# Kernel optimization log

Measured on AMD Instinct MI355X. Metric: run time of the kernel, lower is better.

## Reference

```python
import jax, jax.numpy as jnp
import numpy as np

CLIP_LIMIT = 10.0
NTILES = 8        # OpenCV createCLAHE default tileGridSize=(8,8)
NBINS = 256

_M_RGB2XYZ = jnp.array([[0.412453, 0.357580, 0.180423],
                        [0.212671, 0.715160, 0.072169],
                        [0.019334, 0.119193, 0.950227]], dtype=jnp.float32)
_M_XYZ2RGB = jnp.array([[ 3.240479, -1.537150, -0.498535],
                        [-0.969256,  1.875992,  0.041556],
                        [ 0.055648, -0.204043,  1.057311]], dtype=jnp.float32)
_WP = jnp.array([0.950456, 1.0, 1.088754], dtype=jnp.float32)  # D65 white point (OpenCV)
_EPS = 0.008856


def rgb2lab(rgb):  # rgb: [H,W,3] in [0,1]
    xyz = jnp.einsum('hwc,dc->hwd', rgb, _M_RGB2XYZ) / _WP
    f = jnp.where(xyz > _EPS, jnp.cbrt(xyz), 7.787 * xyz + 16.0 / 116.0)
    fx, fy, fz = f[..., 0], f[..., 1], f[..., 2]
    L = 116.0 * fy - 16.0
    a = 500.0 * (fx - fy)
    b = 200.0 * (fy - fz)
    return L, a, b


def lab2rgb(L, a, b):
    fy = (L + 16.0) / 116.0
    fx = fy + a / 500.0
    fz = fy - b / 200.0
    f = jnp.stack([fx, fy, fz], axis=-1)
    xyz = jnp.where(f ** 3 > _EPS, f ** 3, (f - 16.0 / 116.0) / 7.787) * _WP
    rgb = jnp.einsum('hwd,cd->hwc', xyz, _M_XYZ2RGB)
    return jnp.clip(rgb, 0.0, 1.0)


def clahe_channel(L8, clip_limit):
    # L8: [H,W] int32 in [0,255]
    H, W = L8.shape
    th, tw = H // NTILES, W // NTILES
    area = float(th * tw)
    # per-tile histograms via one scatter-add
    rows = jnp.arange(H) // th            # [H] tile row id
    cols = jnp.arange(W) // tw            # [W] tile col id
    tid = rows[:, None] * NTILES + cols[None, :]          # [H,W]
    flat = (tid * NBINS + L8).ravel()
    hist = jnp.zeros(NTILES * NTILES * NBINS, jnp.float32).at[flat].add(1.0)
    hist = hist.reshape(NTILES * NTILES, NBINS)
    # clip + uniform redistribution of excess
    clip = max(clip_limit * area / NBINS, 1.0)
    excess = jnp.sum(jnp.maximum(hist - clip, 0.0), axis=1, keepdims=True)
    hist = jnp.minimum(hist, clip) + excess / NBINS
    # CDF -> LUT (OpenCV: lutScale = 255/tileArea, rounded)
    cdf = jnp.cumsum(hist, axis=1)
    lut = jnp.clip(jnp.round(cdf * (255.0 / area)), 0.0, 255.0)  # [T, 256]
    # bilinear interpolation between tile LUTs
    fy = jnp.clip((jnp.arange(H, dtype=jnp.float32) + 0.5) / th - 0.5, 0.0, NTILES - 1.0)
    fx = jnp.clip((jnp.arange(W, dtype=jnp.float32) + 0.5) / tw - 0.5, 0.0, NTILES - 1.0)
    y0 = jnp.floor(fy).astype(jnp.int32); y1 = jnp.minimum(y0 + 1, NTILES - 1)
    x0 = jnp.floor(fx).astype(jnp.int32); x1 = jnp.minimum(x0 + 1, NTILES - 1)
    wy = (fy - y0)[:, None]; wx = (fx - x0)[None, :]
    def g(yi, xi):  # gather LUT value for each pixel from tile (yi, xi)
        return lut[yi[:, None] * NTILES + xi[None, :], L8]
    top = (1.0 - wx) * g(y0, x0) + wx * g(y0, x1)
    bot = (1.0 - wx) * g(y1, x0) + wx * g(y1, x1)
    return (1.0 - wy) * top + wy * bot   # [H,W] float in [0,255]


def setup_inputs() -> dict:
    key = jax.random.key(0)
    x = jax.random.uniform(key, (3, 2048, 2048), dtype=jnp.float32)
    return {"x": x}


def reference(x) -> jnp.ndarray:
    hwc = jnp.transpose(x, (1, 2, 0))          # CHW -> HWC
    L, a, b = rgb2lab(hwc)                      # L in [0,100]
    L8 = jnp.clip(jnp.round(L * (255.0 / 100.0)), 0, 255).astype(jnp.int32)
    L_eq = clahe_channel(L8, CLIP_LIMIT) * (100.0 / 255.0)
    rgb = lab2rgb(L_eq, a, b)
    return jnp.transpose(rgb, (2, 0, 1))        # HWC -> CHW
```

## Files before the change

### kernel.cpp

```cpp
#include <hip/hip_runtime.h>
#include <stdint.h>

#define HW 4194304
#define WIDTH 2048
#define F(x) ((float)(x))

__device__ __forceinline__ float cbrtf_glibc(float x) {
    unsigned int bits = __float_as_uint(x);
    int xe = (int)((bits >> 23) & 0xFF) - 126;
    float xm = __uint_as_float((bits & 0x007FFFFFu) | 0x3F000000u);

    static const double factor[5] = {
        1.0 / 1.5874010519681994748,
        1.0 / 1.2599210498948731648,
        1.0,
        1.2599210498948731648,
        1.5874010519681994748
    };

    double xmd = (double)xm;
    double p = __dsub_rn(0.697570460207922770, __dmul_rn(0.191502161678719066, xmd));
    p = __dadd_rn(0.492659620528969547, __dmul_rn(p, xmd));
    float u = (float)p;

    float t2 = __fmul_rn(__fmul_rn(u, u), u);

    double ud  = (double)u;
    double t2d = (double)t2;
    double num = __dmul_rn(ud, __dadd_rn(t2d, __dmul_rn(2.0, xmd)));
    double den = __dadd_rn(__dmul_rn(2.0, t2d), xmd);
    double ym  = __dmul_rn(__ddiv_rn(num, den), factor[2 + (xe % 3)]);
    float ymf = (float)ym;

    return ldexpf(ymf, xe / 3);
}

__device__ __forceinline__ void rgb2lab_px(float r, float g, float b,
                                           int& l8, float& A_, float& B_) {
    float X = __fadd_rn(__fadd_rn(__fmul_rn(r, F(0.412453)), __fmul_rn(g, F(0.357580))), __fmul_rn(b, F(0.180423)));
    float Y = __fadd_rn(__fadd_rn(__fmul_rn(r, F(0.212671)), __fmul_rn(g, F(0.715160))), __fmul_rn(b, F(0.072169)));
    float Z = __fadd_rn(__fadd_rn(__fmul_rn(r, F(0.019334)), __fmul_rn(g, F(0.119193))), __fmul_rn(b, F(0.950227)));
    X = __fdiv_rn(X, F(0.950456));
    Z = __fdiv_rn(Z, F(1.088754));
    const float EPS = F(0.008856);
    const float C0  = F(16.0 / 116.0);
    float fx = (X > EPS) ? cbrtf_glibc(X) : __fadd_rn(__fmul_rn(F(7.787), X), C0);
    float fy = (Y > EPS) ? cbrtf_glibc(Y) : __fadd_rn(__fmul_rn(F(7.787), Y), C0);
    float fz = (Z > EPS) ? cbrtf_glibc(Z) : __fadd_rn(__fmul_rn(F(7.787), Z), C0);
    float L  = __fsub_rn(__fmul_rn(F(116.0), fy), F(16.0));
    A_ = __fmul_rn(F(500.0), __fsub_rn(fx, fy));
    B_ = __fmul_rn(F(200.0), __fsub_rn(fy, fz));
    float Lr = rintf(__fmul_rn(L, F(255.0 / 100.0)));
    Lr = fminf(fmaxf(Lr, 0.0f), 255.0f);
    l8 = (int)Lr;
}

__global__ __launch_bounds__(256) void k_hist(const float* __restrict__ x,
        unsigned int* __restrict__ hist,
        float2* __restrict__ ab_out,
        unsigned char* __restrict__ l8_out, int store) {
    __shared__ unsigned int h[2048];
    const int t = threadIdx.x;
    const int y = blockIdx.x;
    #pragma unroll
    for (int i = 0; i < 8; ++i) h[i * 256 + t] = 0;
    __syncthreads();
    const float* R  = x;
    const float* G  = x + HW;
    const float* Bp = x + 2 * HW;
    const int rowbase = y * WIDTH;
    #pragma unroll
    for (int c = 0; c < 8; ++c) {
        int col = c * 256 + t;
        int idx = rowbase + col;
        float r = R[idx], g = G[idx], b = Bp[idx];
        int l8; float A_, B_;
        rgb2lab_px(r, g, b, l8, A_, B_);
        if (store) {
            ab_out[idx] = make_float2(A_, B_);
            l8_out[idx] = (unsigned char)l8;
        }
        atomicAdd(&h[((col >> 8) << 8) + l8], 1u);
    }
    __syncthreads();
    const int tilerow = y >> 8;
    unsigned int* gh = hist + tilerow * 2048;
    #pragma unroll
    for (int i = 0; i < 8; ++i) {
        unsigned int v = h[i * 256 + t];
        if (v) atomicAdd(&gh[i * 256 + t], v);
    }
}

__global__ __launch_bounds__(256) void k_lut(const unsigned int* __restrict__ hist,
                                             float* __restrict__ lut) {
    __shared__ float sh[256];
    __shared__ float hc[256];
    const int t = threadIdx.x;
    const int tile = blockIdx.x;
    float h = (float)hist[tile * 256 + t];
    sh[t] = fmaxf(h - 2560.0f, 0.0f);
    __syncthreads();
    for (int s = 128; s > 0; s >>= 1) {
        if (t < s) sh[t] += sh[t + s];
        __syncthreads();
    }
    float excess = sh[0];
    hc[t] = __fadd_rn(fminf(h, 2560.0f), __fmul_rn(excess, F(1.0 / 256.0)));
    __syncthreads();
    if (t == 0) {
        float c = 0.0f;
        for (int i = 0; i < 256; ++i) { c = __fadd_rn(c, hc[i]); hc[i] = c; }
    }
    __syncthreads();
    float v = rintf(__fmul_rn(hc[t], F(255.0 / 65536.0)));
    lut[tile * 256 + t] = fminf(fmaxf(v, 0.0f), 255.0f);
}

__global__ __launch_bounds__(256) void k_apply(const float* __restrict__ x,
        const float* __restrict__ lut,
        const float2* __restrict__ ab_in,
        const unsigned char* __restrict__ l8_in,
        float* __restrict__ out, int stored) {
    __shared__ float lutS[4096];
    const int t = threadIdx.x;
    const int y = blockIdx.x;

    float fyc = fminf(fmaxf(((float)y + 0.5f) * (1.0f / 256.0f) - 0.5f, 0.0f), 7.0f);
    int y0 = (int)floorf(fyc); int y1 = min(y0 + 1, 7);
    float wy = __fsub_rn(fyc, (float)y0);
    float omwy = __fsub_rn(1.0f, wy);

    const float* ltop = lut + y0 * 2048;
    const float* lbot = lut + y1 * 2048;
    #pragma unroll
    for (int i = 0; i < 8; ++i) {
        lutS[i * 256 + t]        = ltop[i * 256 + t];
        lutS[2048 + i * 256 + t] = lbot[i * 256 + t];
    }
    __syncthreads();

    const int rowbase = y * WIDTH;
    #pragma unroll
    for (int c = 0; c < 8; ++c) {
        int col = c * 256 + t;
        int idx = rowbase + col;
        int l8; float A_, B_;
        if (stored) {
            float2 ab = ab_in[idx];
            A_ = ab.x; B_ = ab.y;
            l8 = (int)l8_in[idx];
        } else {
            float r = x[idx], g = x[idx + HW], b = x[idx + 2 * HW];
            rgb2lab_px(r, g, b, l8, A_, B_);
        }
        float fxc = fminf(fmaxf(((float)col + 0.5f) * (1.0f / 256.0f) - 0.5f, 0.0f), 7.0f);
        int x0 = (int)floorf(fxc); int x1 = min(x0 + 1, 7);
        float wx = __fsub_rn(fxc, (float)x0);
        float omwx = __fsub_rn(1.0f, wx);
        float g00 = lutS[x0 * 256 + l8];
        float g01 = lutS[x1 * 256 + l8];
        float g10 = lutS[2048 + x0 * 256 + l8];
        float g11 = lutS[2048 + x1 * 256 + l8];
        float top = __fadd_rn(__fmul_rn(omwx, g00), __fmul_rn(wx, g01));
        float bot = __fadd_rn(__fmul_rn(omwx, g10), __fmul_rn(wx, g11));
        float Leq = __fmul_rn(__fadd_rn(__fmul_rn(omwy, top), __fmul_rn(wy, bot)),
                              F(100.0 / 255.0));
        const float EPS = F(0.008856);
        const float C0  = F(16.0 / 116.0);
        float fy2 = __fdiv_rn(__fadd_rn(Leq, 16.0f), 116.0f);
        float fx2 = __fadd_rn(fy2, __fdiv_rn(A_, 500.0f));
        float fz2 = __fsub_rn(fy2, __fdiv_rn(B_, 200.0f));
        float t3;
        t3 = fx2 * fx2 * fx2;
        float X = ((t3 > EPS) ? t3 : __fdiv_rn(__fsub_rn(fx2, C0), F(7.787))) * F(0.950456);
        t3 = fy2 * fy2 * fy2;
        float Y = ((t3 > EPS) ? t3 : __fdiv_rn(__fsub_rn(fy2, C0), F(7.787))) * F(1.0);
        t3 = fz2 * fz2 * fz2;
        float Z = ((t3 > EPS) ? t3 : __fdiv_rn(__fsub_rn(fz2, C0), F(7.787))) * F(1.088754);
        float rr = __fadd_rn(__fadd_rn(__fmul_rn(X, F(3.240479)),  __fmul_rn(Y, F(-1.537150))), __fmul_rn(Z, F(-0.498535)));
        float gg = __fadd_rn(__fadd_rn(__fmul_rn(X, F(-0.969256)), __fmul_rn(Y, F(1.875992))),  __fmul_rn(Z, F(0.041556)));
        float bb = __fadd_rn(__fadd_rn(__fmul_rn(X, F(0.055648)),  __fmul_rn(Y, F(-0.204043))), __fmul_rn(Z, F(1.057311)));
        rr = fminf(fmaxf(rr, 0.0f), 1.0f);
        gg = fminf(fmaxf(gg, 0.0f), 1.0f);
        bb = fminf(fmaxf(bb, 0.0f), 1.0f);
        out[idx]          = rr;
        out[idx + HW]     = gg;
        out[idx + 2 * HW] = bb;
    }
}

extern "C" void kernel_launch(void* const* d_in, const int* in_sizes, int n_in,
                              void* d_out, int out_size, void* d_ws, size_t ws_size,
                              hipStream_t stream) {
    const float* x = (const float*)d_in[0];
    float* out = (float*)d_out;
    char* ws = (char*)d_ws;
    unsigned int* hist = (unsigned int*)ws;
    float* lut = (float*)(ws + 65536);
    const size_t off = 131072;
    float2* ab_buf = (float2*)(ws + off);
    unsigned char* l8_buf = (unsigned char*)(ws + off + (size_t)HW * 8);
    const size_t need = off + (size_t)HW * 9;
    const int store = (ws_size >= need) ? 1 : 0;

    (void)hipMemsetAsync(hist, 0, 65536, stream);
    k_hist<<<2048, 256, 0, stream>>>(x, hist, ab_buf, l8_buf, store);
    k_lut<<<64, 256, 0, stream>>>(hist, lut);
    k_apply<<<2048, 256, 0, stream>>>(x, lut, ab_buf, l8_buf, out, store);
}
```

Measured before the change: 134.4 us.

## Fuse histogram, LUT and apply into one cooperative kernel with register-held Lab

Replaces the three-kernel pipeline with a single cooperative kernel of 1024 blocks. Each block handles two rows and keeps the a/b values and packed L8 in registers across two grid-wide syncs, so the 36 MB intermediate write and re-read through the workspace disappears. The LUT prefix sum becomes a parallel Hillis-Steele scan instead of a serial loop. In exchange it adds grid-sync cost and register pressure under launch_bounds(256,4), and depends on all 1024 blocks being co-resident, falling back to the old path otherwise.

```diff
diff --git a/kernel.cpp b/kernel.cpp
--- a/kernel.cpp
+++ b/kernel.cpp
@@ -1,5 +1,8 @@
 #include <hip/hip_runtime.h>
+#include <hip/hip_cooperative_groups.h>
 #include <stdint.h>
+
+namespace cg = cooperative_groups;
 
 #define HW 4194304
 #define WIDTH 2048
@@ -55,6 +58,153 @@
     l8 = (int)Lr;
 }
 
+__device__ __forceinline__ void lab2rgb_store(float Leq, float A_, float B_,
+                                              float* __restrict__ out, int idx) {
+    const float EPS = F(0.008856);
+    const float C0  = F(16.0 / 116.0);
+    float fy2 = __fdiv_rn(__fadd_rn(Leq, 16.0f), 116.0f);
+    float fx2 = __fadd_rn(fy2, __fdiv_rn(A_, 500.0f));
+    float fz2 = __fsub_rn(fy2, __fdiv_rn(B_, 200.0f));
+    float t3;
+    t3 = fx2 * fx2 * fx2;
+    float X = ((t3 > EPS) ? t3 : __fdiv_rn(__fsub_rn(fx2, C0), F(7.787))) * F(0.950456);
+    t3 = fy2 * fy2 * fy2;
+    float Y = ((t3 > EPS) ? t3 : __fdiv_rn(__fsub_rn(fy2, C0), F(7.787))) * F(1.0);
+    t3 = fz2 * fz2 * fz2;
+    float Z = ((t3 > EPS) ? t3 : __fdiv_rn(__fsub_rn(fz2, C0), F(7.787))) * F(1.088754);
+    float rr = __fadd_rn(__fadd_rn(__fmul_rn(X, F(3.240479)),  __fmul_rn(Y, F(-1.537150))), __fmul_rn(Z, F(-0.498535)));
+    float gg = __fadd_rn(__fadd_rn(__fmul_rn(X, F(-0.969256)), __fmul_rn(Y, F(1.875992))),  __fmul_rn(Z, F(0.041556)));
+    float bb = __fadd_rn(__fadd_rn(__fmul_rn(X, F(0.055648)),  __fmul_rn(Y, F(-0.204043))), __fmul_rn(Z, F(1.057311)));
+    rr = fminf(fmaxf(rr, 0.0f), 1.0f);
+    gg = fminf(fmaxf(gg, 0.0f), 1.0f);
+    bb = fminf(fmaxf(bb, 0.0f), 1.0f);
+    out[idx]          = rr;
+    out[idx + HW]     = gg;
+    out[idx + 2 * HW] = bb;
+}
+
+__global__ __launch_bounds__(256, 4) void k_fused(
+        const float* __restrict__ x,
+        unsigned int* __restrict__ hist,
+        float* __restrict__ lut,
+        float* __restrict__ out) {
+    __shared__ float lds[4096];
+    const int t = threadIdx.x;
+    const int b = blockIdx.x;
+    const int r0 = b * 2;
+
+    unsigned int* h = (unsigned int*)lds;
+    #pragma unroll
+    for (int i = 0; i < 8; ++i) h[i * 256 + t] = 0;
+    __syncthreads();
+
+    const float* R  = x;
+    const float* G  = x + HW;
+    const float* Bp = x + 2 * HW;
+
+    float Areg[2][8], Breg[2][8];
+    unsigned int l8p[2][2] = {{0u, 0u}, {0u, 0u}};
+
+    #pragma unroll
+    for (int rr = 0; rr < 2; ++rr) {
+        const int rowbase = (r0 + rr) * WIDTH;
+        #pragma unroll
+        for (int c = 0; c < 8; ++c) {
+            int col = c * 256 + t;
+            int idx = rowbase + col;
+            float r = R[idx], g = G[idx], bb = Bp[idx];
+            int l8; float A_, B_;
+            rgb2lab_px(r, g, bb, l8, A_, B_);
+            Areg[rr][c] = A_;
+            Breg[rr][c] = B_;
+            l8p[rr][c >> 2] |= (unsigned int)l8 << ((c & 3) * 8);
+            atomicAdd(&h[((col >> 8) << 8) + l8], 1u);
+        }
+    }
+    __syncthreads();
+    {
+        const int tilerow = r0 >> 8;
+        unsigned int* gh = hist + tilerow * 2048;
+        #pragma unroll
+        for (int i = 0; i < 8; ++i) {
+            unsigned int v = h[i * 256 + t];
+            if (v) atomicAdd(&gh[i * 256 + t], v);
+        }
+    }
+    __threadfence();
+    cg::this_grid().sync();
+
+    if (b < 64) {
+        float hval = (float)hist[b * 256 + t];
+        float* sh = lds;
+        sh[t] = fmaxf(hval - 2560.0f, 0.0f);
+        __syncthreads();
+        for (int s = 128; s > 0; s >>= 1) {
+            if (t < s) sh[t] += sh[t + s];
+            __syncthreads();
+        }
+        float excess = sh[0];
+        float val = __fadd_rn(fminf(hval, 2560.0f), __fmul_rn(excess, F(1.0 / 256.0)));
+        float* sc = lds + 256;
+        sc[t] = val;
+        __syncthreads();
+        #pragma unroll
+        for (int s = 1; s < 256; s <<= 1) {
+            float add = (t >= s) ? sc[t - s] : 0.0f;
+            __syncthreads();
+            val = __fadd_rn(val, add);
+            sc[t] = val;
+            __syncthreads();
+        }
+        float lv = rintf(__fmul_rn(val, F(255.0 / 65536.0)));
+        lut[b * 256 + t] = fminf(fmaxf(lv, 0.0f), 255.0f);
+    }
+    cg::this_grid().sync();
+
+    float fyc = fminf(fmaxf(((float)r0 + 0.5f) * (1.0f / 256.0f) - 0.5f, 0.0f), 7.0f);
+    int y0 = (int)floorf(fyc);
+    int y1 = min(y0 + 1, 7);
+    const float* ltop = lut + y0 * 2048;
+    const float* lbot = lut + y1 * 2048;
+    #pragma unroll
+    for (int i = 0; i < 8; ++i) {
+        lds[i * 256 + t]        = ltop[i * 256 + t];
+        lds[2048 + i * 256 + t] = lbot[i * 256 + t];
+    }
+    __syncthreads();
+
+    #pragma unroll
+    for (int rr = 0; rr < 2; ++rr) {
+        const int y = r0 + rr;
+        float fyr = fminf(fmaxf(((float)y + 0.5f) * (1.0f / 256.0f) - 0.5f, 0.0f), 7.0f);
+        float wy = __fsub_rn(fyr, (float)y0);
+        float omwy = __fsub_rn(1.0f, wy);
+        const int rowbase = y * WIDTH;
+        #pragma unroll
+        for (int c = 0; c < 8; ++c) {
+            int col = c * 256 + t;
+            int idx = rowbase + col;
+            int l8 = (int)((l8p[rr][c >> 2] >> ((c & 3) * 8)) & 0xFFu);
+            float A_ = Areg[rr][c];
+            float B_ = Breg[rr][c];
+            float fxc = fminf(fmaxf(((float)col + 0.5f) * (1.0f / 256.0f) - 0.5f, 0.0f), 7.0f);
+            int x0 = (int)floorf(fxc);
+            int x1 = min(x0 + 1, 7);
+            float wx = __fsub_rn(fxc, (float)x0);
+            float omwx = __fsub_rn(1.0f, wx);
+            float g00 = lds[x0 * 256 + l8];
+            float g01 = lds[x1 * 256 + l8];
+            float g10 = lds[2048 + x0 * 256 + l8];
+            float g11 = lds[2048 + x1 * 256 + l8];
+            float top = __fadd_rn(__fmul_rn(omwx, g00), __fmul_rn(wx, g01));
+            float bot = __fadd_rn(__fmul_rn(omwx, g10), __fmul_rn(wx, g11));
+            float Leq = __fmul_rn(__fadd_rn(__fmul_rn(omwy, top), __fmul_rn(wy, bot)),
+                                  F(100.0 / 255.0));
+            lab2rgb_store(Leq, A_, B_, out, idx);
+        }
+    }
+}
+
 __global__ __launch_bounds__(256) void k_hist(const float* __restrict__ x,
         unsigned int* __restrict__ hist,
         float2* __restrict__ ab_out,
@@ -166,27 +316,7 @@
         float bot = __fadd_rn(__fmul_rn(omwx, g10), __fmul_rn(wx, g11));
         float Leq = __fmul_rn(__fadd_rn(__fmul_rn(omwy, top), __fmul_rn(wy, bot)),
                               F(100.0 / 255.0));
-        const float EPS = F(0.008856);
-        const float C0  = F(16.0 / 116.0);
-        float fy2 = __fdiv_rn(__fadd_rn(Leq, 16.0f), 116.0f);
-        float fx2 = __fadd_rn(fy2, __fdiv_rn(A_, 500.0f));
-        float fz2 = __fsub_rn(fy2, __fdiv_rn(B_, 200.0f));
-        float t3;
-        t3 = fx2 * fx2 * fx2;
-        float X = ((t3 > EPS) ? t3 : __fdiv_rn(__fsub_rn(fx2, C0), F(7.787))) * F(0.950456);
-        t3 = fy2 * fy2 * fy2;
-        float Y = ((t3 > EPS) ? t3 : __fdiv_rn(__fsub_rn(fy2, C0), F(7.787))) * F(1.0);
-        t3 = fz2 * fz2 * fz2;
-        float Z = ((t3 > EPS) ? t3 : __fdiv_rn(__fsub_rn(fz2, C0), F(7.787))) * F(1.088754);
-        float rr = __fadd_rn(__fadd_rn(__fmul_rn(X, F(3.240479)),  __fmul_rn(Y, F(-1.537150))), __fmul_rn(Z, F(-0.498535)));
-        float gg = __fadd_rn(__fadd_rn(__fmul_rn(X, F(-0.969256)), __fmul_rn(Y, F(1.875992))),  __fmul_rn(Z, F(0.041556)));
-        float bb = __fadd_rn(__fadd_rn(__fmul_rn(X, F(0.055648)),  __fmul_rn(Y, F(-0.204043))), __fmul_rn(Z, F(1.057311)));
-        rr = fminf(fmaxf(rr, 0.0f), 1.0f);
-        gg = fminf(fmaxf(gg, 0.0f), 1.0f);
-        bb = fminf(fmaxf(bb, 0.0f), 1.0f);
-        out[idx]          = rr;
-        out[idx + HW]     = gg;
-        out[idx + 2 * HW] = bb;
+        lab2rgb_store(Leq, A_, B_, out, idx);
     }
 }
 
@@ -198,14 +328,37 @@
     char* ws = (char*)d_ws;
     unsigned int* hist = (unsigned int*)ws;
     float* lut = (float*)(ws + 65536);
-    const size_t off = 131072;
-    float2* ab_buf = (float2*)(ws + off);
-    unsigned char* l8_buf = (unsigned char*)(ws + off + (size_t)HW * 8);
-    const size_t need = off + (size_t)HW * 9;
-    const int store = (ws_size >= need) ? 1 : 0;
+
+    static int coop_state = -1;
+    if (coop_state < 0) {
+        int nb = 0, ncu = 0, dev = 0;
+        (void)hipGetDevice(&dev);
+        hipError_t e1 = hipOccupancyMaxActiveBlocksPerMultiprocessor(&nb, k_fused, 256, 0);
+        hipError_t e2 = hipDeviceGetAttribute(&ncu, hipDeviceAttributeMultiprocessorCount, dev);
+        coop_state = (e1 == hipSuccess && e2 == hipSuccess && nb * ncu >= 1024) ? 1 : 0;
+    }
 
     (void)hipMemsetAsync(hist, 0, 65536, stream);
-    k_hist<<<2048, 256, 0, stream>>>(x, hist, ab_buf, l8_buf, store);
-    k_lut<<<64, 256, 0, stream>>>(hist, lut);
-    k_apply<<<2048, 256, 0, stream>>>(x, lut, ab_buf, l8_buf, out, store);
-}
+
+    bool done = false;
+    if (coop_state == 1) {
+        const float* xa = x; unsigned int* ha = hist; float* la = lut; float* oa = out;
+        void* kargs[] = { (void*)&xa, (void*)&ha, (void*)&la, (void*)&oa };
+        hipError_t le = hipLaunchCooperativeKernel((const void*)k_fused,
+                                                   dim3(1024), dim3(256),
+                                                   kargs, 0u, stream);
+        done = (le == hipSuccess);
+        if (!done) coop_state = 0;
+    }
+
+    if (!done) {
+        const size_t off = 131072;
+        float2* ab_buf = (float2*)(ws + off);
+        unsigned char* l8_buf = (unsigned char*)(ws + off + (size_t)HW * 8);
+        const size_t need = off + (size_t)HW * 9;
+        const int store = (ws_size >= need) ? 1 : 0;
+        k_hist<<<2048, 256, 0, stream>>>(x, hist, ab_buf, l8_buf, store);
+        k_lut<<<64, 256, 0, stream>>>(hist, lut);
+        k_apply<<<2048, 256, 0, stream>>>(x, lut, ab_buf, l8_buf, out, store);
+    }
+}
```

Result: no change. 135.7 us (+0.9%).

## Fuse histogram, LUT, and apply into one persistent kernel with grid barrier

Applied to the files above, without the earlier changes.

Replaces the three-kernel pipeline with a single kernel. Each row block computes Lab in registers, builds its histogram, then waits at a software grid-wide barrier. After the barrier it builds only the two needed tile-row LUTs locally with wave shuffles and applies them without reloading pixels. This removes the intermediate a/b and L8 buffers in global memory and two kernel launches. In exchange it needs all 2048 blocks co-resident, which is checked via occupancy at runtime with a fallback path. Every block also redundantly recomputes 16 tile LUTs, and the spin barrier adds contention.

```diff
diff --git a/kernel.cpp b/kernel.cpp
--- a/kernel.cpp
+++ b/kernel.cpp
@@ -3,6 +3,7 @@
 
 #define HW 4194304
 #define WIDTH 2048
+#define NBLK 2048
 #define F(x) ((float)(x))
 
 __device__ __forceinline__ float cbrtf_glibc(float x) {
@@ -55,6 +56,162 @@
     l8 = (int)Lr;
 }
 
+__device__ __forceinline__ void lab2rgb_store(float Leq, float A_, float B_,
+                                              float* __restrict__ out, int idx) {
+    const float EPS = F(0.008856);
+    const float C0  = F(16.0 / 116.0);
+    float fy2 = __fdiv_rn(__fadd_rn(Leq, 16.0f), 116.0f);
+    float fx2 = __fadd_rn(fy2, __fdiv_rn(A_, 500.0f));
+    float fz2 = __fsub_rn(fy2, __fdiv_rn(B_, 200.0f));
+    float t3;
+    t3 = fx2 * fx2 * fx2;
+    float X = ((t3 > EPS) ? t3 : __fdiv_rn(__fsub_rn(fx2, C0), F(7.787))) * F(0.950456);
+    t3 = fy2 * fy2 * fy2;
+    float Y = ((t3 > EPS) ? t3 : __fdiv_rn(__fsub_rn(fy2, C0), F(7.787))) * F(1.0);
+    t3 = fz2 * fz2 * fz2;
+    float Z = ((t3 > EPS) ? t3 : __fdiv_rn(__fsub_rn(fz2, C0), F(7.787))) * F(1.088754);
+    float rr = __fadd_rn(__fadd_rn(__fmul_rn(X, F(3.240479)),  __fmul_rn(Y, F(-1.537150))), __fmul_rn(Z, F(-0.498535)));
+    float gg = __fadd_rn(__fadd_rn(__fmul_rn(X, F(-0.969256)), __fmul_rn(Y, F(1.875992))),  __fmul_rn(Z, F(0.041556)));
+    float bb = __fadd_rn(__fadd_rn(__fmul_rn(X, F(0.055648)),  __fmul_rn(Y, F(-0.204043))), __fmul_rn(Z, F(1.057311)));
+    rr = fminf(fmaxf(rr, 0.0f), 1.0f);
+    gg = fminf(fmaxf(gg, 0.0f), 1.0f);
+    bb = fminf(fmaxf(bb, 0.0f), 1.0f);
+    out[idx]          = rr;
+    out[idx + HW]     = gg;
+    out[idx + 2 * HW] = bb;
+}
+
+__global__ __launch_bounds__(256, 8) void k_fused_row(
+        const float* __restrict__ x,
+        unsigned int* __restrict__ hist,
+        unsigned int* __restrict__ bar,
+        float* __restrict__ out) {
+    __shared__ float lutS[4096];
+    unsigned int* h = (unsigned int*)lutS;
+    const int t = threadIdx.x;
+    const int y = blockIdx.x;
+
+    #pragma unroll
+    for (int i = 0; i < 8; ++i) h[i * 256 + t] = 0;
+    __syncthreads();
+
+    float A[8], B[8];
+    unsigned int l8p[2] = {0u, 0u};
+    const int rowbase = y * WIDTH;
+    #pragma unroll
+    for (int c = 0; c < 8; ++c) {
+        int col = c * 256 + t;
+        int idx = rowbase + col;
+        float r = x[idx], g = x[idx + HW], b = x[idx + 2 * HW];
+        int l8;
+        rgb2lab_px(r, g, b, l8, A[c], B[c]);
+        l8p[c >> 2] |= (unsigned int)l8 << ((c & 3) * 8);
+        atomicAdd(&h[((col >> 8) << 8) + l8], 1u);
+    }
+    __syncthreads();
+    {
+        unsigned int* gh = hist + (y >> 8) * 2048;
+        #pragma unroll
+        for (int i = 0; i < 8; ++i) {
+            unsigned int v = h[i * 256 + t];
+            if (v) atomicAdd(&gh[i * 256 + t], v);
+        }
+    }
+
+    __syncthreads();
+    if (t == 0) {
+        __threadfence();
+        unsigned int arrived = __hip_atomic_fetch_add(&bar[0], 1u,
+                                   __ATOMIC_ACQ_REL, __HIP_MEMORY_SCOPE_AGENT);
+        if (arrived == NBLK - 1) {
+            __hip_atomic_store(&bar[1], 1u, __ATOMIC_RELEASE, __HIP_MEMORY_SCOPE_AGENT);
+        } else {
+            for (long it = 0; it < (1L << 26); ++it) {
+                if (__hip_atomic_load(&bar[1], __ATOMIC_ACQUIRE,
+                                      __HIP_MEMORY_SCOPE_AGENT) != 0u) break;
+                __builtin_amdgcn_s_sleep(2);
+            }
+        }
+    }
+    __syncthreads();
+
+    float fyc = fminf(fmaxf(((float)y + 0.5f) * (1.0f / 256.0f) - 0.5f, 0.0f), 7.0f);
+    int y0 = (int)floorf(fyc);
+    int y1 = min(y0 + 1, 7);
+    float wy = __fsub_rn(fyc, (float)y0);
+    float omwy = __fsub_rn(1.0f, wy);
+
+    {
+        const int lane = t & 63;
+        const int w = t >> 6;
+        #pragma unroll
+        for (int i = 0; i < 4; ++i) {
+            int gidx = w * 4 + i;
+            int trow = gidx >> 3;
+            int tcol = gidx & 7;
+            int tile = (trow ? y1 : y0) * 8 + tcol;
+            const unsigned int* hp = hist + tile * 256 + lane * 4;
+            float h0 = (float)__hip_atomic_load(&hp[0], __ATOMIC_RELAXED, __HIP_MEMORY_SCOPE_AGENT);
+            float h1 = (float)__hip_atomic_load(&hp[1], __ATOMIC_RELAXED, __HIP_MEMORY_SCOPE_AGENT);
+            float h2 = (float)__hip_atomic_load(&hp[2], __ATOMIC_RELAXED, __HIP_MEMORY_SCOPE_AGENT);
+            float h3 = (float)__hip_atomic_load(&hp[3], __ATOMIC_RELAXED, __HIP_MEMORY_SCOPE_AGENT);
+            float e = __fadd_rn(__fadd_rn(fmaxf(h0 - 2560.0f, 0.0f),
+                                          fmaxf(h1 - 2560.0f, 0.0f)),
+                                __fadd_rn(fmaxf(h2 - 2560.0f, 0.0f),
+                                          fmaxf(h3 - 2560.0f, 0.0f)));
+            #pragma unroll
+            for (int d = 1; d < 64; d <<= 1) e = __fadd_rn(e, __shfl_xor(e, d));
+            float ex = __fmul_rn(e, F(1.0 / 256.0));
+            float v0 = __fadd_rn(fminf(h0, 2560.0f), ex);
+            float v1 = __fadd_rn(fminf(h1, 2560.0f), ex);
+            float v2 = __fadd_rn(fminf(h2, 2560.0f), ex);
+            float v3 = __fadd_rn(fminf(h3, 2560.0f), ex);
+            float s0 = v0;
+            float s1 = __fadd_rn(s0, v1);
+            float s2 = __fadd_rn(s1, v2);
+            float s3 = __fadd_rn(s2, v3);
+            float sc = s3;
+            #pragma unroll
+            for (int d = 1; d < 64; d <<= 1) {
+                float u2 = __shfl_up(sc, d);
+                if (lane >= d) sc = __fadd_rn(sc, u2);
+            }
+            float excl = __fsub_rn(sc, s3);
+            int base = trow * 2048 + tcol * 256 + lane * 4;
+            float c0 = rintf(__fmul_rn(__fadd_rn(excl, s0), F(255.0 / 65536.0)));
+            float c1 = rintf(__fmul_rn(__fadd_rn(excl, s1), F(255.0 / 65536.0)));
+            float c2 = rintf(__fmul_rn(__fadd_rn(excl, s2), F(255.0 / 65536.0)));
+            float c3 = rintf(__fmul_rn(__fadd_rn(excl, s3), F(255.0 / 65536.0)));
+            lutS[base + 0] = fminf(fmaxf(c0, 0.0f), 255.0f);
+            lutS[base + 1] = fminf(fmaxf(c1, 0.0f), 255.0f);
+            lutS[base + 2] = fminf(fmaxf(c2, 0.0f), 255.0f);
+            lutS[base + 3] = fminf(fmaxf(c3, 0.0f), 255.0f);
+        }
+    }
+    __syncthreads();
+
+    #pragma unroll
+    for (int c = 0; c < 8; ++c) {
+        int col = c * 256 + t;
+        int idx = rowbase + col;
+        int l8 = (int)((l8p[c >> 2] >> ((c & 3) * 8)) & 0xFFu);
+        float fxc = fminf(fmaxf(((float)col + 0.5f) * (1.0f / 256.0f) - 0.5f, 0.0f), 7.0f);
+        int x0 = (int)floorf(fxc);
+        int x1 = min(x0 + 1, 7);
+        float wx = __fsub_rn(fxc, (float)x0);
+        float omwx = __fsub_rn(1.0f, wx);
+        float g00 = lutS[x0 * 256 + l8];
+        float g01 = lutS[x1 * 256 + l8];
+        float g10 = lutS[2048 + x0 * 256 + l8];
+        float g11 = lutS[2048 + x1 * 256 + l8];
+        float top = __fadd_rn(__fmul_rn(omwx, g00), __fmul_rn(wx, g01));
+        float bot = __fadd_rn(__fmul_rn(omwx, g10), __fmul_rn(wx, g11));
+        float Leq = __fmul_rn(__fadd_rn(__fmul_rn(omwy, top), __fmul_rn(wy, bot)),
+                              F(100.0 / 255.0));
+        lab2rgb_store(Leq, A[c], B[c], out, idx);
+    }
+}
+
 __global__ __launch_bounds__(256) void k_hist(const float* __restrict__ x,
         unsigned int* __restrict__ hist,
         float2* __restrict__ ab_out,
@@ -65,15 +222,12 @@
     #pragma unroll
     for (int i = 0; i < 8; ++i) h[i * 256 + t] = 0;
     __syncthreads();
-    const float* R  = x;
-    const float* G  = x + HW;
-    const float* Bp = x + 2 * HW;
     const int rowbase = y * WIDTH;
     #pragma unroll
     for (int c = 0; c < 8; ++c) {
         int col = c * 256 + t;
         int idx = rowbase + col;
-        float r = R[idx], g = G[idx], b = Bp[idx];
+        float r = x[idx], g = x[idx + HW], b = x[idx + 2 * HW];
         int l8; float A_, B_;
         rgb2lab_px(r, g, b, l8, A_, B_);
         if (store) {
@@ -166,27 +320,7 @@
         float bot = __fadd_rn(__fmul_rn(omwx, g10), __fmul_rn(wx, g11));
         float Leq = __fmul_rn(__fadd_rn(__fmul_rn(omwy, top), __fmul_rn(wy, bot)),
                               F(100.0 / 255.0));
-        const float EPS = F(0.008856);
-        const float C0  = F(16.0 / 116.0);
-        float fy2 = __fdiv_rn(__fadd_rn(Leq, 16.0f), 116.0f);
-        float fx2 = __fadd_rn(fy2, __fdiv_rn(A_, 500.0f));
-        float fz2 = __fsub_rn(fy2, __fdiv_rn(B_, 200.0f));
-        float t3;
-        t3 = fx2 * fx2 * fx2;
-        float X = ((t3 > EPS) ? t3 : __fdiv_rn(__fsub_rn(fx2, C0), F(7.787))) * F(0.950456);
-        t3 = fy2 * fy2 * fy2;
-        float Y = ((t3 > EPS) ? t3 : __fdiv_rn(__fsub_rn(fy2, C0), F(7.787))) * F(1.0);
-        t3 = fz2 * fz2 * fz2;
-        float Z = ((t3 > EPS) ? t3 : __fdiv_rn(__fsub_rn(fz2, C0), F(7.787))) * F(1.088754);
-        float rr = __fadd_rn(__fadd_rn(__fmul_rn(X, F(3.240479)),  __fmul_rn(Y, F(-1.537150))), __fmul_rn(Z, F(-0.498535)));
-        float gg = __fadd_rn(__fadd_rn(__fmul_rn(X, F(-0.969256)), __fmul_rn(Y, F(1.875992))),  __fmul_rn(Z, F(0.041556)));
-        float bb = __fadd_rn(__fadd_rn(__fmul_rn(X, F(0.055648)),  __fmul_rn(Y, F(-0.204043))), __fmul_rn(Z, F(1.057311)));
-        rr = fminf(fmaxf(rr, 0.0f), 1.0f);
-        gg = fminf(fmaxf(gg, 0.0f), 1.0f);
-        bb = fminf(fmaxf(bb, 0.0f), 1.0f);
-        out[idx]          = rr;
-        out[idx + HW]     = gg;
-        out[idx + 2 * HW] = bb;
+        lab2rgb_store(Leq, A_, B_, out, idx);
     }
 }
 
@@ -197,15 +331,30 @@
     float* out = (float*)d_out;
     char* ws = (char*)d_ws;
     unsigned int* hist = (unsigned int*)ws;
+    unsigned int* bar  = (unsigned int*)(ws + 65536);
     float* lut = (float*)(ws + 65536);
-    const size_t off = 131072;
-    float2* ab_buf = (float2*)(ws + off);
-    unsigned char* l8_buf = (unsigned char*)(ws + off + (size_t)HW * 8);
-    const size_t need = off + (size_t)HW * 9;
-    const int store = (ws_size >= need) ? 1 : 0;
-
-    (void)hipMemsetAsync(hist, 0, 65536, stream);
-    k_hist<<<2048, 256, 0, stream>>>(x, hist, ab_buf, l8_buf, store);
-    k_lut<<<64, 256, 0, stream>>>(hist, lut);
-    k_apply<<<2048, 256, 0, stream>>>(x, lut, ab_buf, l8_buf, out, store);
-}
+
+    static int fused_ok = -1;
+    if (fused_ok < 0) {
+        int nb = 0, ncu = 0, dev = 0;
+        (void)hipGetDevice(&dev);
+        hipError_t e1 = hipOccupancyMaxActiveBlocksPerMultiprocessor(&nb, k_fused_row, 256, 0);
+        hipError_t e2 = hipDeviceGetAttribute(&ncu, hipDeviceAttributeMultiprocessorCount, dev);
+        fused_ok = (e1 == hipSuccess && e2 == hipSuccess && nb * ncu >= NBLK) ? 1 : 0;
+    }
+
+    (void)hipMemsetAsync(ws, 0, 65536 + 64, stream);
+
+    if (fused_ok == 1) {
+        k_fused_row<<<NBLK, 256, 0, stream>>>(x, hist, bar, out);
+    } else {
+        const size_t off = 131072;
+        float2* ab_buf = (float2*)(ws + off);
+        unsigned char* l8_buf = (unsigned char*)(ws + off + (size_t)HW * 8);
+        const size_t need = off + (size_t)HW * 9;
+        const int store = (ws_size >= need) ? 1 : 0;
+        k_hist<<<2048, 256, 0, stream>>>(x, hist, ab_buf, l8_buf, store);
+        k_lut<<<64, 256, 0, stream>>>(hist, lut);
+        k_apply<<<2048, 256, 0, stream>>>(x, lut, ab_buf, l8_buf, out, store);
+    }
+}
```

New measurement: 134.1 us. Within noise of the previous version (-0.2%).

## Drop intermediate ab/L8 buffers, recompute Lab in apply, fuse LUT build

Applied to the files above, without the earlier changes.

The histogram pass now computes only luminance and no longer writes the a/b and L8 intermediates to workspace. The apply pass re-reads RGB and recomputes Lab. Each apply block builds its two tile-row LUTs directly from the histograms with wavefront shuffle reductions and scans, which removes the separate LUT kernel. Loads and stores are vectorised to float4 with 8 pixels per thread. This cuts about 36 MB of intermediate traffic and one launch, at the cost of recomputing the cube roots and redundantly rebuilding LUTs in every block.

```diff
diff --git a/kernel.cpp b/kernel.cpp
--- a/kernel.cpp
+++ b/kernel.cpp
@@ -55,36 +55,68 @@
     l8 = (int)Lr;
 }
 
-__global__ __launch_bounds__(256) void k_hist(const float* __restrict__ x,
-        unsigned int* __restrict__ hist,
-        float2* __restrict__ ab_out,
-        unsigned char* __restrict__ l8_out, int store) {
+__device__ __forceinline__ int l8_of_rgb(float r, float g, float b) {
+    float Y = __fadd_rn(__fadd_rn(__fmul_rn(r, F(0.212671)), __fmul_rn(g, F(0.715160))), __fmul_rn(b, F(0.072169)));
+    const float EPS = F(0.008856);
+    const float C0  = F(16.0 / 116.0);
+    float fy = (Y > EPS) ? cbrtf_glibc(Y) : __fadd_rn(__fmul_rn(F(7.787), Y), C0);
+    float L  = __fsub_rn(__fmul_rn(F(116.0), fy), F(16.0));
+    float Lr = rintf(__fmul_rn(L, F(255.0 / 100.0)));
+    Lr = fminf(fmaxf(Lr, 0.0f), 255.0f);
+    return (int)Lr;
+}
+
+__device__ __forceinline__ void lab2rgb_px(float Leq, float A_, float B_,
+                                           float& rr, float& gg, float& bb) {
+    const float EPS = F(0.008856);
+    const float C0  = F(16.0 / 116.0);
+    float fy2 = __fdiv_rn(__fadd_rn(Leq, 16.0f), 116.0f);
+    float fx2 = __fadd_rn(fy2, __fdiv_rn(A_, 500.0f));
+    float fz2 = __fsub_rn(fy2, __fdiv_rn(B_, 200.0f));
+    float t3;
+    t3 = fx2 * fx2 * fx2;
+    float X = ((t3 > EPS) ? t3 : __fdiv_rn(__fsub_rn(fx2, C0), F(7.787))) * F(0.950456);
+    t3 = fy2 * fy2 * fy2;
+    float Y = ((t3 > EPS) ? t3 : __fdiv_rn(__fsub_rn(fy2, C0), F(7.787))) * F(1.0);
+    t3 = fz2 * fz2 * fz2;
+    float Z = ((t3 > EPS) ? t3 : __fdiv_rn(__fsub_rn(fz2, C0), F(7.787))) * F(1.088754);
+    rr = __fadd_rn(__fadd_rn(__fmul_rn(X, F(3.240479)),  __fmul_rn(Y, F(-1.537150))), __fmul_rn(Z, F(-0.498535)));
+    gg = __fadd_rn(__fadd_rn(__fmul_rn(X, F(-0.969256)), __fmul_rn(Y, F(1.875992))),  __fmul_rn(Z, F(0.041556)));
+    bb = __fadd_rn(__fadd_rn(__fmul_rn(X, F(0.055648)),  __fmul_rn(Y, F(-0.204043))), __fmul_rn(Z, F(1.057311)));
+    rr = fminf(fmaxf(rr, 0.0f), 1.0f);
+    gg = fminf(fmaxf(gg, 0.0f), 1.0f);
+    bb = fminf(fmaxf(bb, 0.0f), 1.0f);
+}
+
+__global__ __launch_bounds__(256, 4) void k_histY(const float* __restrict__ x,
+                                                  unsigned int* __restrict__ hist) {
     __shared__ unsigned int h[2048];
     const int t = threadIdx.x;
     const int y = blockIdx.x;
     #pragma unroll
     for (int i = 0; i < 8; ++i) h[i * 256 + t] = 0;
     __syncthreads();
-    const float* R  = x;
-    const float* G  = x + HW;
-    const float* Bp = x + 2 * HW;
-    const int rowbase = y * WIDTH;
-    #pragma unroll
-    for (int c = 0; c < 8; ++c) {
-        int col = c * 256 + t;
-        int idx = rowbase + col;
-        float r = R[idx], g = G[idx], b = Bp[idx];
-        int l8; float A_, B_;
-        rgb2lab_px(r, g, b, l8, A_, B_);
-        if (store) {
-            ab_out[idx] = make_float2(A_, B_);
-            l8_out[idx] = (unsigned char)l8;
-        }
-        atomicAdd(&h[((col >> 8) << 8) + l8], 1u);
-    }
+
+    const int base = y * WIDTH + t * 8;
+    float4 ra = *(const float4*)(x + base);
+    float4 rb = *(const float4*)(x + base + 4);
+    float4 ga = *(const float4*)(x + base + HW);
+    float4 gb = *(const float4*)(x + base + HW + 4);
+    float4 ba = *(const float4*)(x + base + 2 * HW);
+    float4 bb = *(const float4*)(x + base + 2 * HW + 4);
+
+    const int hb = ((t >> 5) << 8);
+    atomicAdd(&h[hb + l8_of_rgb(ra.x, ga.x, ba.x)], 1u);
+    atomicAdd(&h[hb + l8_of_rgb(ra.y, ga.y, ba.y)], 1u);
+    atomicAdd(&h[hb + l8_of_rgb(ra.z, ga.z, ba.z)], 1u);
+    atomicAdd(&h[hb + l8_of_rgb(ra.w, ga.w, ba.w)], 1u);
+    atomicAdd(&h[hb + l8_of_rgb(rb.x, gb.x, bb.x)], 1u);
+    atomicAdd(&h[hb + l8_of_rgb(rb.y, gb.y, bb.y)], 1u);
+    atomicAdd(&h[hb + l8_of_rgb(rb.z, gb.z, bb.z)], 1u);
+    atomicAdd(&h[hb + l8_of_rgb(rb.w, gb.w, bb.w)], 1u);
+
     __syncthreads();
-    const int tilerow = y >> 8;
-    unsigned int* gh = hist + tilerow * 2048;
+    unsigned int* gh = hist + (y >> 8) * 2048;
     #pragma unroll
     for (int i = 0; i < 8; ++i) {
         unsigned int v = h[i * 256 + t];
@@ -92,102 +124,112 @@
     }
 }
 
-__global__ __launch_bounds__(256) void k_lut(const unsigned int* __restrict__ hist,
-                                             float* __restrict__ lut) {
-    __shared__ float sh[256];
-    __shared__ float hc[256];
-    const int t = threadIdx.x;
-    const int tile = blockIdx.x;
-    float h = (float)hist[tile * 256 + t];
-    sh[t] = fmaxf(h - 2560.0f, 0.0f);
-    __syncthreads();
-    for (int s = 128; s > 0; s >>= 1) {
-        if (t < s) sh[t] += sh[t + s];
-        __syncthreads();
-    }
-    float excess = sh[0];
-    hc[t] = __fadd_rn(fminf(h, 2560.0f), __fmul_rn(excess, F(1.0 / 256.0)));
-    __syncthreads();
-    if (t == 0) {
-        float c = 0.0f;
-        for (int i = 0; i < 256; ++i) { c = __fadd_rn(c, hc[i]); hc[i] = c; }
-    }
-    __syncthreads();
-    float v = rintf(__fmul_rn(hc[t], F(255.0 / 65536.0)));
-    lut[tile * 256 + t] = fminf(fmaxf(v, 0.0f), 255.0f);
-}
-
-__global__ __launch_bounds__(256) void k_apply(const float* __restrict__ x,
-        const float* __restrict__ lut,
-        const float2* __restrict__ ab_in,
-        const unsigned char* __restrict__ l8_in,
-        float* __restrict__ out, int stored) {
+__global__ __launch_bounds__(256, 4) void k_lut_apply(const float* __restrict__ x,
+        const unsigned int* __restrict__ hist,
+        float* __restrict__ out) {
     __shared__ float lutS[4096];
     const int t = threadIdx.x;
     const int y = blockIdx.x;
 
     float fyc = fminf(fmaxf(((float)y + 0.5f) * (1.0f / 256.0f) - 0.5f, 0.0f), 7.0f);
-    int y0 = (int)floorf(fyc); int y1 = min(y0 + 1, 7);
+    int y0 = (int)floorf(fyc);
+    int y1 = min(y0 + 1, 7);
     float wy = __fsub_rn(fyc, (float)y0);
     float omwy = __fsub_rn(1.0f, wy);
 
-    const float* ltop = lut + y0 * 2048;
-    const float* lbot = lut + y1 * 2048;
-    #pragma unroll
-    for (int i = 0; i < 8; ++i) {
-        lutS[i * 256 + t]        = ltop[i * 256 + t];
-        lutS[2048 + i * 256 + t] = lbot[i * 256 + t];
+    {
+        const int lane = t & 63;
+        const int w = t >> 6;
+        #pragma unroll
+        for (int i = 0; i < 4; ++i) {
+            int gidx = w * 4 + i;
+            int trow = gidx >> 3;
+            int tcol = gidx & 7;
+            int tile = (trow ? y1 : y0) * 8 + tcol;
+            uint4 hv = *(const uint4*)(hist + tile * 256 + lane * 4);
+            float h0 = (float)hv.x, h1 = (float)hv.y, h2 = (float)hv.z, h3 = (float)hv.w;
+            float e = __fadd_rn(__fadd_rn(fmaxf(h0 - 2560.0f, 0.0f),
+                                          fmaxf(h1 - 2560.0f, 0.0f)),
+                                __fadd_rn(fmaxf(h2 - 2560.0f, 0.0f),
+                                          fmaxf(h3 - 2560.0f, 0.0f)));
+            #pragma unroll
+            for (int d = 1; d < 64; d <<= 1) e = __fadd_rn(e, __shfl_xor(e, d));
+            float ex = __fmul_rn(e, F(1.0 / 256.0));
+            float v0 = __fadd_rn(fminf(h0, 2560.0f), ex);
+            float v1 = __fadd_rn(fminf(h1, 2560.0f), ex);
+            float v2 = __fadd_rn(fminf(h2, 2560.0f), ex);
+            float v3 = __fadd_rn(fminf(h3, 2560.0f), ex);
+            float s0 = v0;
+            float s1 = __fadd_rn(s0, v1);
+            float s2 = __fadd_rn(s1, v2);
+            float s3 = __fadd_rn(s2, v3);
+            float sc = s3;
+            #pragma unroll
+            for (int d = 1; d < 64; d <<= 1) {
+                float u2 = __shfl_up(sc, d);
+                if (lane >= d) sc = __fadd_rn(sc, u2);
+            }
+            float excl = __fsub_rn(sc, s3);
+            int lb = trow * 2048 + tcol * 256 + lane * 4;
+            float c0 = rintf(__fmul_rn(__fadd_rn(excl, s0), F(255.0 / 65536.0)));
+            float c1 = rintf(__fmul_rn(__fadd_rn(excl, s1), F(255.0 / 65536.0)));
+            float c2 = rintf(__fmul_rn(__fadd_rn(excl, s2), F(255.0 / 65536.0)));
+            float c3 = rintf(__fmul_rn(__fadd_rn(excl, s3), F(255.0 / 65536.0)));
+            lutS[lb + 0] = fminf(fmaxf(c0, 0.0f), 255.0f);
+            lutS[lb + 1] = fminf(fmaxf(c1, 0.0f), 255.0f);
+            lutS[lb + 2] = fminf(fmaxf(c2, 0.0f), 255.0f);
+            lutS[lb + 3] = fminf(fmaxf(c3, 0.0f), 255.0f);
+        }
     }
     __syncthreads();
 
-    const int rowbase = y * WIDTH;
-    #pragma unroll
-    for (int c = 0; c < 8; ++c) {
-        int col = c * 256 + t;
-        int idx = rowbase + col;
-        int l8; float A_, B_;
-        if (stored) {
-            float2 ab = ab_in[idx];
-            A_ = ab.x; B_ = ab.y;
-            l8 = (int)l8_in[idx];
-        } else {
-            float r = x[idx], g = x[idx + HW], b = x[idx + 2 * HW];
-            rgb2lab_px(r, g, b, l8, A_, B_);
-        }
-        float fxc = fminf(fmaxf(((float)col + 0.5f) * (1.0f / 256.0f) - 0.5f, 0.0f), 7.0f);
-        int x0 = (int)floorf(fxc); int x1 = min(x0 + 1, 7);
-        float wx = __fsub_rn(fxc, (float)x0);
-        float omwx = __fsub_rn(1.0f, wx);
-        float g00 = lutS[x0 * 256 + l8];
-        float g01 = lutS[x1 * 256 + l8];
-        float g10 = lutS[2048 + x0 * 256 + l8];
-        float g11 = lutS[2048 + x1 * 256 + l8];
-        float top = __fadd_rn(__fmul_rn(omwx, g00), __fmul_rn(wx, g01));
-        float bot = __fadd_rn(__fmul_rn(omwx, g10), __fmul_rn(wx, g11));
-        float Leq = __fmul_rn(__fadd_rn(__fmul_rn(omwy, top), __fmul_rn(wy, bot)),
-                              F(100.0 / 255.0));
-        const float EPS = F(0.008856);
-        const float C0  = F(16.0 / 116.0);
-        float fy2 = __fdiv_rn(__fadd_rn(Leq, 16.0f), 116.0f);
-        float fx2 = __fadd_rn(fy2, __fdiv_rn(A_, 500.0f));
-        float fz2 = __fsub_rn(fy2, __fdiv_rn(B_, 200.0f));
-        float t3;
-        t3 = fx2 * fx2 * fx2;
-        float X = ((t3 > EPS) ? t3 : __fdiv_rn(__fsub_rn(fx2, C0), F(7.787))) * F(0.950456);
-        t3 = fy2 * fy2 * fy2;
-        float Y = ((t3 > EPS) ? t3 : __fdiv_rn(__fsub_rn(fy2, C0), F(7.787))) * F(1.0);
-        t3 = fz2 * fz2 * fz2;
-        float Z = ((t3 > EPS) ? t3 : __fdiv_rn(__fsub_rn(fz2, C0), F(7.787))) * F(1.088754);
-        float rr = __fadd_rn(__fadd_rn(__fmul_rn(X, F(3.240479)),  __fmul_rn(Y, F(-1.537150))), __fmul_rn(Z, F(-0.498535)));
-        float gg = __fadd_rn(__fadd_rn(__fmul_rn(X, F(-0.969256)), __fmul_rn(Y, F(1.875992))),  __fmul_rn(Z, F(0.041556)));
-        float bb = __fadd_rn(__fadd_rn(__fmul_rn(X, F(0.055648)),  __fmul_rn(Y, F(-0.204043))), __fmul_rn(Z, F(1.057311)));
-        rr = fminf(fmaxf(rr, 0.0f), 1.0f);
-        gg = fminf(fmaxf(gg, 0.0f), 1.0f);
-        bb = fminf(fmaxf(bb, 0.0f), 1.0f);
-        out[idx]          = rr;
-        out[idx + HW]     = gg;
-        out[idx + 2 * HW] = bb;
-    }
+    const int colbase = t * 8;
+    const int base = y * WIDTH + colbase;
+    float4 ra = *(const float4*)(x + base);
+    float4 rb = *(const float4*)(x + base + 4);
+    float4 ga = *(const float4*)(x + base + HW);
+    float4 gb = *(const float4*)(x + base + HW + 4);
+    float4 ba = *(const float4*)(x + base + 2 * HW);
+    float4 bb = *(const float4*)(x + base + 2 * HW + 4);
+
+    float4 o_r0, o_r1, o_g0, o_g1, o_b0, o_b1;
+
+#define PIX(RV, GV, BV, J, OR_, OG_, OB_) {                                       \
+    int col = colbase + (J);                                                      \
+    int l8; float A_, B_;                                                         \
+    rgb2lab_px((RV), (GV), (BV), l8, A_, B_);                                     \
+    float fxc = fminf(fmaxf(((float)col + 0.5f) * (1.0f / 256.0f) - 0.5f, 0.0f), 7.0f); \
+    int x0 = (int)floorf(fxc);                                                    \
+    int x1 = min(x0 + 1, 7);                                                      \
+    float wx = __fsub_rn(fxc, (float)x0);                                         \
+    float omwx = __fsub_rn(1.0f, wx);                                             \
+    float g00 = lutS[x0 * 256 + l8];                                              \
+    float g01 = lutS[x1 * 256 + l8];                                              \
+    float g10 = lutS[2048 + x0 * 256 + l8];                                       \
+    float g11 = lutS[2048 + x1 * 256 + l8];                                       \
+    float top_ = __fadd_rn(__fmul_rn(omwx, g00), __fmul_rn(wx, g01));             \
+    float bot_ = __fadd_rn(__fmul_rn(omwx, g10), __fmul_rn(wx, g11));             \
+    float Leq = __fmul_rn(__fadd_rn(__fmul_rn(omwy, top_), __fmul_rn(wy, bot_)),  \
+                          F(100.0 / 255.0));                                      \
+    lab2rgb_px(Leq, A_, B_, (OR_), (OG_), (OB_));                                 \
+}
+
+    PIX(ra.x, ga.x, ba.x, 0, o_r0.x, o_g0.x, o_b0.x);
+    PIX(ra.y, ga.y, ba.y, 1, o_r0.y, o_g0.y, o_b0.y);
+    PIX(ra.z, ga.z, ba.z, 2, o_r0.z, o_g0.z, o_b0.z);
+    PIX(ra.w, ga.w, ba.w, 3, o_r0.w, o_g0.w, o_b0.w);
+    PIX(rb.x, gb.x, bb.x, 4, o_r1.x, o_g1.x, o_b1.x);
+    PIX(rb.y, gb.y, bb.y, 5, o_r1.y, o_g1.y, o_b1.y);
+    PIX(rb.z, gb.z, bb.z, 6, o_r1.z, o_g1.z, o_b1.z);
+    PIX(rb.w, gb.w, bb.w, 7, o_r1.w, o_g1.w, o_b1.w);
+#undef PIX
+
+    *(float4*)(out + base)              = o_r0;
+    *(float4*)(out + base + 4)          = o_r1;
+    *(float4*)(out + base + HW)         = o_g0;
+    *(float4*)(out + base + HW + 4)     = o_g1;
+    *(float4*)(out + base + 2 * HW)     = o_b0;
+    *(float4*)(out + base + 2 * HW + 4) = o_b1;
 }
 
 extern "C" void kernel_launch(void* const* d_in, const int* in_sizes, int n_in,
@@ -195,17 +237,9 @@
                               hipStream_t stream) {
     const float* x = (const float*)d_in[0];
     float* out = (float*)d_out;
-    char* ws = (char*)d_ws;
-    unsigned int* hist = (unsigned int*)ws;
-    float* lut = (float*)(ws + 65536);
-    const size_t off = 131072;
-    float2* ab_buf = (float2*)(ws + off);
-    unsigned char* l8_buf = (unsigned char*)(ws + off + (size_t)HW * 8);
-    const size_t need = off + (size_t)HW * 9;
-    const int store = (ws_size >= need) ? 1 : 0;
+    unsigned int* hist = (unsigned int*)d_ws;
 
     (void)hipMemsetAsync(hist, 0, 65536, stream);
-    k_hist<<<2048, 256, 0, stream>>>(x, hist, ab_buf, l8_buf, store);
-    k_lut<<<64, 256, 0, stream>>>(hist, lut);
-    k_apply<<<2048, 256, 0, stream>>>(x, lut, ab_buf, l8_buf, out, store);
-}
+    k_histY<<<2048, 256, 0, stream>>>(x, hist);
+    k_lut_apply<<<2048, 256, 0, stream>>>(x, hist, out);
+}
```

Measured after the change: 141.8 us. 5.5% more time.
